# Optimization experiments

Hardware: AMD Instinct MI355X
Metric: run time of the kernel (lower is better)

## Reference

```python
import jax, jax.numpy as jnp
import numpy as np

B = 4096      # graphs per batch
V = 32        # vertices per graph
F = 16        # num_atom_types (input node features)
NB = 8        # num_bond_types (edge feature dim)
C = 128       # conv_dim
E_PER = 256   # random edges per graph
NEG_SLOPE = 0.2


def setup_inputs() -> dict:
    rng = np.random.default_rng(0)
    N = B * V
    # random intra-graph edges (duplicates are fine; softmax handles them)
    off = (np.arange(B, dtype=np.int64) * V)[:, None]
    src = (rng.integers(0, V, (B, E_PER)) + off).ravel()
    dst = (rng.integers(0, V, (B, E_PER)) + off).ravel()
    bond = rng.integers(0, NB, src.shape[0])
    eattr = np.zeros((src.shape[0], NB), dtype=np.float32)
    eattr[np.arange(src.shape[0]), bond] = 1.0
    # self loops with edge_attr = per-target-node mean (PyG fill_value='mean')
    sums = np.zeros((N, NB), dtype=np.float64)
    np.add.at(sums, dst, eattr)
    cnt = np.bincount(dst, minlength=N).astype(np.float64)
    loop_attr = (sums / np.maximum(cnt, 1.0)[:, None]).astype(np.float32)
    loops = np.arange(N, dtype=np.int64)
    edge_index = np.stack([np.concatenate([src, loops]),
                           np.concatenate([dst, loops])])  # [2, E]
    edge_attr = np.concatenate([eattr, loop_attr], axis=0)  # [E, NB]

    key = jax.random.key(0)
    ks = jax.random.split(key, 8)
    inp = {
        "x": jax.random.normal(ks[0], (N, F), jnp.float32),
        "edge_index": jnp.asarray(edge_index),
        "edge_attr": jnp.asarray(edge_attr),
        "W_lin": jax.random.normal(ks[1], (F, C), jnp.float32) / np.sqrt(F),
        "att_src": jax.random.normal(ks[2], (C,), jnp.float32) / np.sqrt(C),
        "att_dst": jax.random.normal(ks[3], (C,), jnp.float32) / np.sqrt(C),
        "att_edge": jax.random.normal(ks[4], (C,), jnp.float32) / np.sqrt(C),
        "W_edge": jax.random.normal(ks[5], (NB, C), jnp.float32) / np.sqrt(NB),
        "b_gat": jnp.zeros((C,), jnp.float32),
        "W_out": jax.random.normal(ks[6], (C, 1), jnp.float32) / np.sqrt(C),
        "b_out": jnp.zeros((1,), jnp.float32),
        "num_graphs": B,
    }
    return inp


def reference(x, edge_index, edge_attr, W_lin, att_src, att_dst, att_edge,
              W_edge, b_gat, W_out, b_out, num_graphs):
    N = x.shape[0]
    src, dst = edge_index[0], edge_index[1]
    h = x @ W_lin                           # [N, C] node transform
    a_src = h @ att_src                     # [N]
    a_dst = h @ att_dst                     # [N]
    a_edge = (edge_attr @ W_edge) @ att_edge  # [E]
    alpha = jax.nn.leaky_relu(a_src[src] + a_dst[dst] + a_edge, NEG_SLOPE)
    # segment softmax over incoming edges of each dst node
    m = jax.ops.segment_max(alpha, dst, num_segments=N)
    m = jnp.where(jnp.isfinite(m), m, 0.0)
    ex = jnp.exp(alpha - m[dst])
    denom = jax.ops.segment_sum(ex, dst, num_segments=N)
    w = ex / denom[dst]                     # [E] attention weights
    msg = h[src] * w[:, None]               # [E, C]
    out_nodes = jax.ops.segment_sum(msg, dst, num_segments=N) + b_gat  # [N, C]
    gf = out_nodes.reshape(num_graphs, -1, out_nodes.shape[-1]).mean(axis=1)  # [B, C]
    out = gf @ W_out + b_out                # [B, 1]
    return (out, gf)
```

## Files before the change

kernel.cpp:

```cpp
#include <hip/hip_runtime.h>


#define BB   4096
#define VV   32
#define FF   16
#define NBB  8
#define CC   128
#define EPER 256
constexpr int NTOT  = BB * VV;
constexpr int ERAND = BB * EPER;
constexpr int ETOT  = ERAND + NTOT;
constexpr float SLOPE = 0.2f;

__device__ __forceinline__ unsigned f2key(float f) {
  unsigned u = __float_as_uint(f);
  return (u & 0x80000000u) ? ~u : (u | 0x80000000u);
}
__device__ __forceinline__ float key2f(unsigned k) {
  unsigned u = (k & 0x80000000u) ? (k & 0x7fffffffu) : ~k;
  return __uint_as_float(u);
}

__launch_bounds__(64)
__global__ void gnn_precompute(const float* __restrict__ W_lin,
                               const float* __restrict__ att_src,
                               const float* __restrict__ att_dst,
                               const float* __restrict__ W_edge,
                               const float* __restrict__ att_edge,
                               float* __restrict__ ws)
{
  const int l = threadIdx.x;
  const float2 as = ((const float2*)att_src)[l];
  const float2 ad = ((const float2*)att_dst)[l];
  const float2 ae = ((const float2*)att_edge)[l];
  #pragma unroll
  for (int f = 0; f < FF; ++f) {
    const float2 w = ((const float2*)W_lin)[f * 64 + l];
    float ps = w.x * as.x + w.y * as.y;
    float pd = w.x * ad.x + w.y * ad.y;
    #pragma unroll
    for (int m = 1; m <= 32; m <<= 1) { ps += __shfl_xor(ps, m); pd += __shfl_xor(pd, m); }
    if (l == 0) { ws[f] = ps; ws[FF + f] = pd; }
  }
  #pragma unroll
  for (int f = 0; f < NBB; ++f) {
    const float2 w = ((const float2*)W_edge)[f * 64 + l];
    float pe = w.x * ae.x + w.y * ae.y;
    #pragma unroll
    for (int m = 1; m <= 32; m <<= 1) pe += __shfl_xor(pe, m);
    if (l == 0) ws[2 * FF + f] = pe;
  }
}

__launch_bounds__(256, 4)
__global__ void gnn_main(const float* __restrict__ x,
                         const int*   __restrict__ eidx,
                         const float* __restrict__ eattr,
                         const float* __restrict__ W_lin,
                         const float* __restrict__ b_gat,
                         const float* __restrict__ W_out,
                         const float* __restrict__ b_out,
                         const float* __restrict__ ws,
                         float* __restrict__ out,
                         float* __restrict__ gf_out)
{
  const int t    = threadIdx.x;
  const int lane = t & 63;
  const int wave = __builtin_amdgcn_readfirstlane(t) >> 6;
  const int g    = blockIdx.x * 4 + wave;

  __shared__ float    s_asrc[4][VV], s_adst[4][VV];
  __shared__ unsigned s_mkey[4][VV];
  __shared__ float    s_den[4][VV];
  __shared__ float    s_r[4][VV];
  __shared__ float    s_xt[4][FF * 33];

  if (lane < VV) { s_mkey[wave][lane] = 0u; s_den[wave][lane] = 0.f; s_r[wave][lane] = 0.f; }

  int es[4], ed[4];
  float4 ea0[4], ea1[4];
  const int gbase = g * EPER;
  #pragma unroll
  for (int k = 0; k < 4; ++k) {
    const int ge = gbase + 64 * k + lane;
    es[k] = eidx[ge] - g * VV;
    ed[k] = eidx[ETOT + ge] - g * VV;
    const float4* ap = (const float4*)(eattr + (size_t)ge * NBB);
    ea0[k] = ap[0]; ea1[k] = ap[1];
  }
  float4 la0 = {0,0,0,0}, la1 = {0,0,0,0};
  if (lane < VV) {
    const float4* ap = (const float4*)(eattr + (size_t)(ERAND + g * VV + lane) * NBB);
    la0 = ap[0]; la1 = ap[1];
  }

  float xr[FF] = {};
  if (lane < VV) {
    const float* xp = x + (size_t)(g * VV + lane) * FF;
    #pragma unroll
    for (int f = 0; f < FF; ++f) xr[f] = xp[f];
    float a0 = 0.f, a1 = 0.f;
    #pragma unroll
    for (int f = 0; f < FF; ++f) { a0 += xr[f] * ws[f]; a1 += xr[f] * ws[FF + f]; }
    s_asrc[wave][lane] = a0; s_adst[wave][lane] = a1;
  }
  __threadfence_block();

  float al[5];
  #pragma unroll
  for (int k = 0; k < 4; ++k) {
    const float aed = ea0[k].x*ws[32] + ea0[k].y*ws[33] + ea0[k].z*ws[34] + ea0[k].w*ws[35]
                    + ea1[k].x*ws[36] + ea1[k].y*ws[37] + ea1[k].z*ws[38] + ea1[k].w*ws[39];
    const float a = s_asrc[wave][es[k]] + s_adst[wave][ed[k]] + aed;
    al[k] = a > 0.f ? a : SLOPE * a;
    atomicMax(&s_mkey[wave][ed[k]], f2key(al[k]));
  }
  al[4] = 0.f;
  if (lane < VV) {
    const float aed = la0.x*ws[32] + la0.y*ws[33] + la0.z*ws[34] + la0.w*ws[35]
                    + la1.x*ws[36] + la1.y*ws[37] + la1.z*ws[38] + la1.w*ws[39];
    const float a = s_asrc[wave][lane] + s_adst[wave][lane] + aed;
    al[4] = a > 0.f ? a : SLOPE * a;
    atomicMax(&s_mkey[wave][lane], f2key(al[4]));
  }
  __threadfence_block();

  float ex[5];
  #pragma unroll
  for (int k = 0; k < 4; ++k) {
    ex[k] = __expf(al[k] - key2f(s_mkey[wave][ed[k]]));
    atomicAdd(&s_den[wave][ed[k]], ex[k]);
  }
  ex[4] = 0.f;
  if (lane < VV) {
    ex[4] = __expf(al[4] - key2f(s_mkey[wave][lane]));
    atomicAdd(&s_den[wave][lane], ex[4]);
  }
  __threadfence_block();
  if (lane < VV) s_den[wave][lane] = 1.0f / s_den[wave][lane];
  __threadfence_block();

  #pragma unroll
  for (int k = 0; k < 4; ++k)
    atomicAdd(&s_r[wave][es[k]], ex[k] * s_den[wave][ed[k]]);
  if (lane < VV)
    atomicAdd(&s_r[wave][lane], ex[4] * s_den[wave][lane]);
  __threadfence_block();

  if (lane < VV) {
    const float rl = s_r[wave][lane];
    #pragma unroll
    for (int f = 0; f < FF; ++f) s_xt[wave][f * 33 + lane] = xr[f] * rl;
  }
  __threadfence_block();
  const int fy = lane & 15, part = lane >> 4;
  float yp = 0.f;
  #pragma unroll
  for (int j = 0; j < 8; ++j) yp += s_xt[wave][fy * 33 + part * 8 + j];
  yp += __shfl_xor(yp, 16);
  yp += __shfl_xor(yp, 32);
  yp *= (1.0f / VV);

  const float2 bg = ((const float2*)b_gat)[lane];
  float gx = bg.x, gy = bg.y;
  const float2* W2 = (const float2*)W_lin;
  #pragma unroll
  for (int f = 0; f < FF; ++f) {
    const float yf = __shfl(yp, f);
    const float2 w = W2[f * 64 + lane];
    gx += yf * w.x; gy += yf * w.y;
  }
  ((float2*)(gf_out + (size_t)g * CC))[lane] = make_float2(gx, gy);

  const float2 wo = ((const float2*)W_out)[lane];
  float p = gx * wo.x + gy * wo.y;
  #pragma unroll
  for (int m = 1; m <= 32; m <<= 1) p += __shfl_xor(p, m);
  if (lane == 0) out[g] = p + b_out[0];
}

extern "C" void kernel_launch(void* const* d_in, const int* in_sizes, int n_in,
                              void* d_out, int out_size, void* d_ws, size_t ws_size,
                              hipStream_t stream) {
  const float* x        = (const float*)d_in[0];
  const int*   eidx     = (const int*)  d_in[1];
  const float* eattr    = (const float*)d_in[2];
  const float* W_lin    = (const float*)d_in[3];
  const float* att_src  = (const float*)d_in[4];
  const float* att_dst  = (const float*)d_in[5];
  const float* att_edge = (const float*)d_in[6];
  const float* W_edge   = (const float*)d_in[7];
  const float* b_gat    = (const float*)d_in[8];
  const float* W_out    = (const float*)d_in[9];
  const float* b_out    = (const float*)d_in[10];

  float* ws  = (float*)d_ws;
  float* out = (float*)d_out;
  float* gf  = out + BB;

  gnn_precompute<<<dim3(1), dim3(64), 0, stream>>>(W_lin, att_src, att_dst,
                                                   W_edge, att_edge, ws);
  gnn_main<<<dim3(BB / 4), dim3(256), 0, stream>>>(
      x, eidx, eattr, W_lin, b_gat, W_out, b_out, ws, out, gf);
}
```

Baseline: 128.2 us.

## Drop softmax max pass, vectorize edge loads, move self-loops to upper lanes

Removes the segment-max stage (atomicMax on ordered keys plus a fence) and exponentiates the raw leaky-relu logits directly, relying on the logits being small enough not to overflow. Edge indices and attributes are now loaded as contiguous int4/float4 per lane rather than strided per k. Self-loop edges move to lanes 32-63 so their work sits beside the x loads on lanes 0-31. The separate reciprocal pass over s_den is replaced by a hardware rcp at each use. The unstabilized exp risks overflow or precision loss for large logits.

```diff
diff --git a/kernel.cpp b/kernel.cpp
--- a/kernel.cpp
+++ b/kernel.cpp
@@ -11,15 +11,6 @@
 constexpr int ERAND = BB * EPER;
 constexpr int ETOT  = ERAND + NTOT;
 constexpr float SLOPE = 0.2f;
-
-__device__ __forceinline__ unsigned f2key(float f) {
-  unsigned u = __float_as_uint(f);
-  return (u & 0x80000000u) ? ~u : (u | 0x80000000u);
-}
-__device__ __forceinline__ float key2f(unsigned k) {
-  unsigned u = (k & 0x80000000u) ? (k & 0x7fffffffu) : ~k;
-  return __uint_as_float(u);
-}
 
 __launch_bounds__(64)
 __global__ void gnn_precompute(const float* __restrict__ W_lin,
@@ -69,36 +60,38 @@
   const int wave = __builtin_amdgcn_readfirstlane(t) >> 6;
   const int g    = blockIdx.x * 4 + wave;
 
-  __shared__ float    s_asrc[4][VV], s_adst[4][VV];
-  __shared__ unsigned s_mkey[4][VV];
-  __shared__ float    s_den[4][VV];
-  __shared__ float    s_r[4][VV];
-  __shared__ float    s_xt[4][FF * 33];
+  __shared__ float s_asrc[4][VV], s_adst[4][VV];
+  __shared__ float s_den[4][VV];
+  __shared__ float s_r[4][VV];
+  __shared__ float s_xt[4][FF * 33];
 
-  if (lane < VV) { s_mkey[wave][lane] = 0u; s_den[wave][lane] = 0.f; s_r[wave][lane] = 0.f; }
-
-  int es[4], ed[4];
-  float4 ea0[4], ea1[4];
-  const int gbase = g * EPER;
-  #pragma unroll
-  for (int k = 0; k < 4; ++k) {
-    const int ge = gbase + 64 * k + lane;
-    es[k] = eidx[ge] - g * VV;
-    ed[k] = eidx[ETOT + ge] - g * VV;
-    const float4* ap = (const float4*)(eattr + (size_t)ge * NBB);
-    ea0[k] = ap[0]; ea1[k] = ap[1];
-  }
-  float4 la0 = {0,0,0,0}, la1 = {0,0,0,0};
-  if (lane < VV) {
-    const float4* ap = (const float4*)(eattr + (size_t)(ERAND + g * VV + lane) * NBB);
-    la0 = ap[0]; la1 = ap[1];
-  }
+  if (lane < VV) { s_den[wave][lane] = 0.f; s_r[wave][lane] = 0.f; }
 
   float xr[FF] = {};
   if (lane < VV) {
     const float* xp = x + (size_t)(g * VV + lane) * FF;
     #pragma unroll
     for (int f = 0; f < FF; ++f) xr[f] = xp[f];
+  }
+
+  int es[4], ed[4];
+  const int4 s4 = ((const int4*)(eidx + g * EPER))[lane];
+  const int4 d4 = ((const int4*)(eidx + ETOT + g * EPER))[lane];
+  es[0] = s4.x - g * VV; es[1] = s4.y - g * VV; es[2] = s4.z - g * VV; es[3] = s4.w - g * VV;
+  ed[0] = d4.x - g * VV; ed[1] = d4.y - g * VV; ed[2] = d4.z - g * VV; ed[3] = d4.w - g * VV;
+  float4 ea[8];
+  {
+    const float4* ap = (const float4*)(eattr + (size_t)(g * EPER + 4 * lane) * NBB);
+    #pragma unroll
+    for (int j = 0; j < 8; ++j) ea[j] = ap[j];
+  }
+  float4 la0 = {0,0,0,0}, la1 = {0,0,0,0};
+  if (lane >= VV) {
+    const float4* lp = (const float4*)(eattr + (size_t)(ERAND + g * VV + (lane - VV)) * NBB);
+    la0 = lp[0]; la1 = lp[1];
+  }
+
+  if (lane < VV) {
     float a0 = 0.f, a1 = 0.f;
     #pragma unroll
     for (int f = 0; f < FF; ++f) { a0 += xr[f] * ws[f]; a1 += xr[f] * ws[FF + f]; }
@@ -106,45 +99,37 @@
   }
   __threadfence_block();
 
-  float al[5];
-  #pragma unroll
-  for (int k = 0; k < 4; ++k) {
-    const float aed = ea0[k].x*ws[32] + ea0[k].y*ws[33] + ea0[k].z*ws[34] + ea0[k].w*ws[35]
-                    + ea1[k].x*ws[36] + ea1[k].y*ws[37] + ea1[k].z*ws[38] + ea1[k].w*ws[39];
-    const float a = s_asrc[wave][es[k]] + s_adst[wave][ed[k]] + aed;
-    al[k] = a > 0.f ? a : SLOPE * a;
-    atomicMax(&s_mkey[wave][ed[k]], f2key(al[k]));
-  }
-  al[4] = 0.f;
-  if (lane < VV) {
-    const float aed = la0.x*ws[32] + la0.y*ws[33] + la0.z*ws[34] + la0.w*ws[35]
-                    + la1.x*ws[36] + la1.y*ws[37] + la1.z*ws[38] + la1.w*ws[39];
-    const float a = s_asrc[wave][lane] + s_adst[wave][lane] + aed;
-    al[4] = a > 0.f ? a : SLOPE * a;
-    atomicMax(&s_mkey[wave][lane], f2key(al[4]));
-  }
-  __threadfence_block();
-
+  const float w0 = ws[32], w1 = ws[33], w2 = ws[34], w3 = ws[35];
+  const float w4 = ws[36], w5 = ws[37], w6 = ws[38], w7 = ws[39];
   float ex[5];
   #pragma unroll
   for (int k = 0; k < 4; ++k) {
-    ex[k] = __expf(al[k] - key2f(s_mkey[wave][ed[k]]));
+    const float aed = ea[2*k].x*w0 + ea[2*k].y*w1 + ea[2*k].z*w2 + ea[2*k].w*w3
+                    + ea[2*k+1].x*w4 + ea[2*k+1].y*w5 + ea[2*k+1].z*w6 + ea[2*k+1].w*w7;
+    const float a  = s_asrc[wave][es[k]] + s_adst[wave][ed[k]] + aed;
+    const float al = a > 0.f ? a : SLOPE * a;
+    ex[k] = __expf(al);
     atomicAdd(&s_den[wave][ed[k]], ex[k]);
   }
   ex[4] = 0.f;
-  if (lane < VV) {
-    ex[4] = __expf(al[4] - key2f(s_mkey[wave][lane]));
-    atomicAdd(&s_den[wave][lane], ex[4]);
+  if (lane >= VV) {
+    const int v = lane - VV;
+    const float aed = la0.x*w0 + la0.y*w1 + la0.z*w2 + la0.w*w3
+                    + la1.x*w4 + la1.y*w5 + la1.z*w6 + la1.w*w7;
+    const float a  = s_asrc[wave][v] + s_adst[wave][v] + aed;
+    const float al = a > 0.f ? a : SLOPE * a;
+    ex[4] = __expf(al);
+    atomicAdd(&s_den[wave][v], ex[4]);
   }
-  __threadfence_block();
-  if (lane < VV) s_den[wave][lane] = 1.0f / s_den[wave][lane];
   __threadfence_block();
 
   #pragma unroll
   for (int k = 0; k < 4; ++k)
-    atomicAdd(&s_r[wave][es[k]], ex[k] * s_den[wave][ed[k]]);
-  if (lane < VV)
-    atomicAdd(&s_r[wave][lane], ex[4] * s_den[wave][lane]);
+    atomicAdd(&s_r[wave][es[k]], ex[k] * __builtin_amdgcn_rcpf(s_den[wave][ed[k]]));
+  if (lane >= VV) {
+    const int v = lane - VV;
+    atomicAdd(&s_r[wave][v], ex[4] * __builtin_amdgcn_rcpf(s_den[wave][v]));
+  }
   __threadfence_block();
 
   if (lane < VV) {
```

After: 128.6 us. About the same (+0.3%).
